# Kernel tuning notes

Measured on AMD Instinct MI355X. Metric: run time of the kernel, lower is better.

## Reference

```python
import jax, jax.numpy as jnp
import numpy as np

B, C, H, W = 8, 1, 64, 64


def setup_inputs() -> dict:
    key = jax.random.key(0)
    ks = jax.random.split(key, 7)
    return {
        "x": jax.random.normal(ks[0], (B, C, H, W), dtype=jnp.float32),
        "wq": jax.random.normal(ks[1], (), dtype=jnp.float32),
        "bq": jax.random.normal(ks[2], (), dtype=jnp.float32),
        "wk": jax.random.normal(ks[3], (), dtype=jnp.float32),
        "bk": jax.random.normal(ks[4], (), dtype=jnp.float32),
        "wv": jax.random.normal(ks[5], (), dtype=jnp.float32),
        "bv": jax.random.normal(ks[6], (), dtype=jnp.float32),
        "gamma": jnp.zeros((), dtype=jnp.float32),
    }


def reference(x, wq, bq, wk, bk, wv, bv, gamma):
    b, c, h, w = x.shape
    n = h * w  # number of spatial tokens
    xf = x.reshape(b, n)  # channels == 1, so flatten spatial dims
    # 1x1 conv with 1->1 channels is a scalar affine per pixel
    q = wq * xf + bq  # [B, N]
    k = wk * xf + bk  # [B, N]
    v = wv * xf + bv  # [B, N]
    # scores[b,i,j] = q_i * k_j (no sqrt(d) scaling in the original)
    scores = jnp.einsum("bn,bm->bnm", q, k)  # [B, N, N]
    attn = jax.nn.softmax(scores, axis=-1)
    # out_i = sum_j attn[i,j] * v_j  (torch: bmm(v, attn^T))
    out = jnp.einsum("bnm,bm->bn", attn, v)  # [B, N]
    return gamma * out.reshape(b, c, h, w) + x
```

## Files before the change

### kernel.cpp

```cpp
#include <hip/hip_runtime.h>


#define N_TOK   4096
#define NB      8
#define KN      64
#define LOG2E   1.4426950408889634f
#define PI_F    3.14159265358979323846f

__device__ __forceinline__ float fast_exp2(float v) { return __builtin_amdgcn_exp2f(v); }
__device__ __forceinline__ float fast_rcp(float v)  { return __builtin_amdgcn_rcpf(v); }

__global__ __launch_bounds__(64) void SelfAttention_nodes_kernel(
    const float* __restrict__ x,
    const float* __restrict__ pwq, const float* __restrict__ pbq,
    const float* __restrict__ pwk,
    float4* __restrict__ tab)
{
    const int lane = threadIdx.x;
    const int b    = blockIdx.x & (NB - 1);
    const int k    = blockIdx.x >> 3;

    const float4* x4 = reinterpret_cast<const float4*>(x + b * N_TOK);
    float4 v[16];
    float mx = -__builtin_inff(), mn = __builtin_inff();
#pragma unroll
    for (int q = 0; q < 16; ++q) {
        v[q] = x4[lane + q * 64];
        mx = fmaxf(mx, fmaxf(fmaxf(v[q].x, v[q].y), fmaxf(v[q].z, v[q].w)));
        mn = fminf(mn, fminf(fminf(v[q].x, v[q].y), fminf(v[q].z, v[q].w)));
    }
#pragma unroll
    for (int m = 32; m >= 1; m >>= 1) {
        mx = fmaxf(mx, __shfl_xor(mx, m, 64));
        mn = fminf(mn, __shfl_xor(mn, m, 64));
    }

    const float wq = *pwq, bq = *pbq, wk = *pwk;

    const float e1  = fmaf(wq, mn, bq) * wk;
    const float e2  = fmaf(wq, mx, bq) * wk;
    const float tlo = fminf(e1, e2), thi = fmaxf(e1, e2);
    const float cc  = 0.5f * (tlo + thi);
    const float rr  = 0.5f * (thi - tlo) * 1.0001f + 1e-7f;

    const float tk = cc + rr * cosf(PI_F * (float)k / (float)(KN - 1));

    const float mshift = fmaxf(tk * mx, tk * mn);
    const float a = tk * LOG2E;
    const float c = mshift * LOG2E;

    float S = 0.f, W = 0.f;
#pragma unroll
    for (int q = 0; q < 16; ++q) {
        float t0 = fast_exp2(fmaf(a, v[q].x, -c));
        float t1 = fast_exp2(fmaf(a, v[q].y, -c));
        float t2 = fast_exp2(fmaf(a, v[q].z, -c));
        float t3 = fast_exp2(fmaf(a, v[q].w, -c));
        S += t0; W = fmaf(t0, v[q].x, W);
        S += t1; W = fmaf(t1, v[q].y, W);
        S += t2; W = fmaf(t2, v[q].z, W);
        S += t3; W = fmaf(t3, v[q].w, W);
    }
#pragma unroll
    for (int m = 32; m >= 1; m >>= 1) {
        S += __shfl_xor(S, m, 64);
        W += __shfl_xor(W, m, 64);
    }

    if (lane == 0) {
        const float g = W / S;
        float wgt = (k == 0 || k == KN - 1) ? 0.5f : 1.0f;
        if (k & 1) wgt = -wgt;
        tab[b * KN + k] = make_float4(tk, wgt, wgt * g, 0.f);
    }
}

__global__ __launch_bounds__(64) void SelfAttention_rows_kernel(
    const float* __restrict__ x,
    const float* __restrict__ pwq, const float* __restrict__ pbq,
    const float* __restrict__ pwk,
    const float* __restrict__ pwv, const float* __restrict__ pbv,
    const float* __restrict__ pgamma,
    const float4* __restrict__ tab,
    float* __restrict__ out)
{
    __shared__ float4 stab[KN];

    const int lane = threadIdx.x;
    const int b    = blockIdx.x & (NB - 1);
    const int blk  = blockIdx.x >> 3;

    stab[lane] = tab[b * KN + lane];
    __syncthreads();

    const float wq = *pwq, bq = *pbq, wk = *pwk;
    const float wv = *pwv, bv = *pbv, gamma = *pgamma;

    const int   i  = blk * 64 + lane;
    const float xi = x[b * N_TOK + i];
    const float t  = fmaf(wq, xi, bq) * wk;

    float num = 0.f, den = 0.f;
#pragma unroll 16
    for (int k = 0; k < KN; ++k) {
        const float4 e = stab[k];
        float d = t - e.x;
        d = copysignf(fmaxf(fabsf(d), 1e-12f), d);
        const float u = fast_rcp(d);
        num = fmaf(u, e.z, num);
        den = fmaf(u, e.y, den);
    }
    const float g = num * fast_rcp(den);
    const float o = fmaf(wv, g, bv);
    out[b * N_TOK + i] = fmaf(gamma, o, xi);
}

extern "C" void kernel_launch(void* const* d_in, const int* in_sizes, int n_in,
                              void* d_out, int out_size, void* d_ws, size_t ws_size,
                              hipStream_t stream) {
    const float* x = (const float*)d_in[0];
    float4* tab = (float4*)d_ws;

    SelfAttention_nodes_kernel<<<dim3(NB * KN), dim3(64), 0, stream>>>(
        x, (const float*)d_in[1], (const float*)d_in[2], (const float*)d_in[3], tab);

    SelfAttention_rows_kernel<<<dim3(NB * (N_TOK / 64)), dim3(64), 0, stream>>>(
        x, (const float*)d_in[1], (const float*)d_in[2], (const float*)d_in[3],
        (const float*)d_in[5], (const float*)d_in[6], (const float*)d_in[7],
        tab, (float*)d_out);
}
```

Before: 72.02 us.

## Fuse node-table and row interpolation kernels into one block-per-batch kernel

Merges the two launches into one kernel where each 1024-thread block loads its batch row into LDS, builds the 64-node interpolation table with a cross-wave reduction, and then evaluates a slice of rows. This removes the second launch and the global-memory round trip for the table. In exchange, each of the 8 blocks per batch recomputes the full table, and only 64 blocks are launched, so much of the GPU sits idle.

```diff
diff --git a/kernel.cpp b/kernel.cpp
--- a/kernel.cpp
+++ b/kernel.cpp
@@ -4,38 +4,58 @@
 #define N_TOK   4096
 #define NB      8
 #define KN      64
+#define BPB     8
+#define ROWS_PB (N_TOK / BPB)
+#define NTHR    1024
+#define NWAVE   (NTHR / 64)
+#define CHUNK   (N_TOK / NWAVE)
 #define LOG2E   1.4426950408889634f
 #define PI_F    3.14159265358979323846f
 
 __device__ __forceinline__ float fast_exp2(float v) { return __builtin_amdgcn_exp2f(v); }
 __device__ __forceinline__ float fast_rcp(float v)  { return __builtin_amdgcn_rcpf(v); }
 
-__global__ __launch_bounds__(64) void SelfAttention_nodes_kernel(
+__global__ __launch_bounds__(NTHR) void SelfAttention_fused_kernel(
     const float* __restrict__ x,
     const float* __restrict__ pwq, const float* __restrict__ pbq,
     const float* __restrict__ pwk,
-    float4* __restrict__ tab)
+    const float* __restrict__ pwv, const float* __restrict__ pbv,
+    const float* __restrict__ pgamma,
+    float* __restrict__ out)
 {
-    const int lane = threadIdx.x;
-    const int b    = blockIdx.x & (NB - 1);
-    const int k    = blockIdx.x >> 3;
+    __shared__ float  sx[N_TOK];
+    __shared__ float4 stab[KN];
+    __shared__ float  sred[2 * NWAVE];
+    __shared__ float  sS[NWAVE][KN];
+    __shared__ float  sW[NWAVE][KN];
+
+    const int tid  = threadIdx.x;
+    const int lane = tid & 63;
+    const int w    = tid >> 6;
+    const int b    = blockIdx.x >> 3;
+    const int blk  = blockIdx.x & (BPB - 1);
+
+    const float wq = *pwq, bq = *pbq, wk = *pwk;
+    const float wv = *pwv, bv = *pbv, gamma = *pgamma;
 
     const float4* x4 = reinterpret_cast<const float4*>(x + b * N_TOK);
-    float4 v[16];
-    float mx = -__builtin_inff(), mn = __builtin_inff();
-#pragma unroll
-    for (int q = 0; q < 16; ++q) {
-        v[q] = x4[lane + q * 64];
-        mx = fmaxf(mx, fmaxf(fmaxf(v[q].x, v[q].y), fmaxf(v[q].z, v[q].w)));
-        mn = fminf(mn, fminf(fminf(v[q].x, v[q].y), fminf(v[q].z, v[q].w)));
-    }
+    const float4 v = x4[tid];
+    reinterpret_cast<float4*>(sx)[tid] = v;
+    float mx = fmaxf(fmaxf(v.x, v.y), fmaxf(v.z, v.w));
+    float mn = fminf(fminf(v.x, v.y), fminf(v.z, v.w));
 #pragma unroll
     for (int m = 32; m >= 1; m >>= 1) {
         mx = fmaxf(mx, __shfl_xor(mx, m, 64));
         mn = fminf(mn, __shfl_xor(mn, m, 64));
     }
-
-    const float wq = *pwq, bq = *pbq, wk = *pwk;
+    if (lane == 0) { sred[w] = mn; sred[NWAVE + w] = mx; }
+    __syncthreads();
+    mn = sred[0]; mx = sred[NWAVE];
+#pragma unroll
+    for (int q = 1; q < NWAVE; ++q) {
+        mn = fminf(mn, sred[q]);
+        mx = fmaxf(mx, sred[NWAVE + q]);
+    }
 
     const float e1  = fmaf(wq, mn, bq) * wk;
     const float e2  = fmaf(wq, mx, bq) * wk;
@@ -43,89 +63,68 @@
     const float cc  = 0.5f * (tlo + thi);
     const float rr  = 0.5f * (thi - tlo) * 1.0001f + 1e-7f;
 
-    const float tk = cc + rr * cosf(PI_F * (float)k / (float)(KN - 1));
-
+    const float tk = cc + rr * cosf(PI_F * (float)lane / (float)(KN - 1));
     const float mshift = fmaxf(tk * mx, tk * mn);
     const float a = tk * LOG2E;
     const float c = mshift * LOG2E;
 
     float S = 0.f, W = 0.f;
-#pragma unroll
-    for (int q = 0; q < 16; ++q) {
-        float t0 = fast_exp2(fmaf(a, v[q].x, -c));
-        float t1 = fast_exp2(fmaf(a, v[q].y, -c));
-        float t2 = fast_exp2(fmaf(a, v[q].z, -c));
-        float t3 = fast_exp2(fmaf(a, v[q].w, -c));
-        S += t0; W = fmaf(t0, v[q].x, W);
-        S += t1; W = fmaf(t1, v[q].y, W);
-        S += t2; W = fmaf(t2, v[q].z, W);
-        S += t3; W = fmaf(t3, v[q].w, W);
+    const float4* xs4 = reinterpret_cast<const float4*>(sx + w * CHUNK);
+#pragma unroll 16
+    for (int i = 0; i < CHUNK / 4; ++i) {
+        const float4 u = xs4[i];
+        const float t0 = fast_exp2(fmaf(a, u.x, -c));
+        const float t1 = fast_exp2(fmaf(a, u.y, -c));
+        const float t2 = fast_exp2(fmaf(a, u.z, -c));
+        const float t3 = fast_exp2(fmaf(a, u.w, -c));
+        S += t0; W = fmaf(t0, u.x, W);
+        S += t1; W = fmaf(t1, u.y, W);
+        S += t2; W = fmaf(t2, u.z, W);
+        S += t3; W = fmaf(t3, u.w, W);
     }
-#pragma unroll
-    for (int m = 32; m >= 1; m >>= 1) {
-        S += __shfl_xor(S, m, 64);
-        W += __shfl_xor(W, m, 64);
-    }
-
-    if (lane == 0) {
-        const float g = W / S;
-        float wgt = (k == 0 || k == KN - 1) ? 0.5f : 1.0f;
-        if (k & 1) wgt = -wgt;
-        tab[b * KN + k] = make_float4(tk, wgt, wgt * g, 0.f);
-    }
-}
-
-__global__ __launch_bounds__(64) void SelfAttention_rows_kernel(
-    const float* __restrict__ x,
-    const float* __restrict__ pwq, const float* __restrict__ pbq,
-    const float* __restrict__ pwk,
-    const float* __restrict__ pwv, const float* __restrict__ pbv,
-    const float* __restrict__ pgamma,
-    const float4* __restrict__ tab,
-    float* __restrict__ out)
-{
-    __shared__ float4 stab[KN];
-
-    const int lane = threadIdx.x;
-    const int b    = blockIdx.x & (NB - 1);
-    const int blk  = blockIdx.x >> 3;
-
-    stab[lane] = tab[b * KN + lane];
+    sS[w][lane] = S;
+    sW[w][lane] = W;
     __syncthreads();
 
-    const float wq = *pwq, bq = *pbq, wk = *pwk;
-    const float wv = *pwv, bv = *pbv, gamma = *pgamma;
+    if (w == 0) {
+        float Ss = 0.f, Ws = 0.f;
+#pragma unroll
+        for (int q = 0; q < NWAVE; ++q) { Ss += sS[q][lane]; Ws += sW[q][lane]; }
+        const float g = Ws / Ss;
+        float wgt = (lane == 0 || lane == KN - 1) ? 0.5f : 1.0f;
+        if (lane & 1) wgt = -wgt;
+        stab[lane] = make_float4(tk, wgt, wgt * g, 0.f);
+    }
+    __syncthreads();
 
-    const int   i  = blk * 64 + lane;
-    const float xi = x[b * N_TOK + i];
-    const float t  = fmaf(wq, xi, bq) * wk;
+    if (tid < ROWS_PB) {
+        const int   i  = blk * ROWS_PB + tid;
+        const float xi = sx[i];
+        const float t  = fmaf(wq, xi, bq) * wk;
 
-    float num = 0.f, den = 0.f;
+        float num = 0.f, den = 0.f;
 #pragma unroll 16
-    for (int k = 0; k < KN; ++k) {
-        const float4 e = stab[k];
-        float d = t - e.x;
-        d = copysignf(fmaxf(fabsf(d), 1e-12f), d);
-        const float u = fast_rcp(d);
-        num = fmaf(u, e.z, num);
-        den = fmaf(u, e.y, den);
+        for (int k = 0; k < KN; ++k) {
+            const float4 e = stab[k];
+            float d = t - e.x;
+            d = copysignf(fmaxf(fabsf(d), 1e-12f), d);
+            const float u = fast_rcp(d);
+            num = fmaf(u, e.z, num);
+            den = fmaf(u, e.y, den);
+        }
+        const float g = num * fast_rcp(den);
+        const float o = fmaf(wv, g, bv);
+        out[b * N_TOK + i] = fmaf(gamma, o, xi);
     }
-    const float g = num * fast_rcp(den);
-    const float o = fmaf(wv, g, bv);
-    out[b * N_TOK + i] = fmaf(gamma, o, xi);
 }
 
 extern "C" void kernel_launch(void* const* d_in, const int* in_sizes, int n_in,
                               void* d_out, int out_size, void* d_ws, size_t ws_size,
                               hipStream_t stream) {
     const float* x = (const float*)d_in[0];
-    float4* tab = (float4*)d_ws;
-
-    SelfAttention_nodes_kernel<<<dim3(NB * KN), dim3(64), 0, stream>>>(
-        x, (const float*)d_in[1], (const float*)d_in[2], (const float*)d_in[3], tab);
-
-    SelfAttention_rows_kernel<<<dim3(NB * (N_TOK / 64)), dim3(64), 0, stream>>>(
-        x, (const float*)d_in[1], (const float*)d_in[2], (const float*)d_in[3],
+    SelfAttention_fused_kernel<<<dim3(NB * BPB), dim3(NTHR), 0, stream>>>(
+        x,
+        (const float*)d_in[1], (const float*)d_in[2], (const float*)d_in[3],
         (const float*)d_in[5], (const float*)d_in[6], (const float*)d_in[7],
-        tab, (float*)d_out);
+        (float*)d_out);
 }
```

Result: slower. 79.53 us (+10.4%).
